# Kernel tuning notes

Hardware: AMD Instinct MI355X
Metric: run time of the kernel (lower is better)

Reference implementation:

```python
import jax, jax.numpy as jnp
import numpy as np

DIM = 2048
H = 16        # num query heads
HK = 2        # num kv heads
D = DIM // H  # head_dim = 128
G = H // HK   # q heads per kv head = 8
SCALE = 1.0 / np.sqrt(D)


def setup_inputs() -> dict:
    key = jax.random.key(0)
    ks = jax.random.split(key, 9)
    xavier = lambda k, fi, fo: jax.random.uniform(k, (fi, fo), jnp.float32,
                                                  -np.sqrt(6.0 / (fi + fo)), np.sqrt(6.0 / (fi + fo)))
    return {
        "x": jax.random.normal(ks[0], (2, 2048, DIM), jnp.float32),
        "Wq": xavier(ks[1], DIM, H * D),  "bq": jnp.zeros((H * D,), jnp.float32),
        "Wk": xavier(ks[2], DIM, HK * D), "bk": jnp.zeros((HK * D,), jnp.float32),
        "Wv": xavier(ks[3], DIM, HK * D), "bv": jnp.zeros((HK * D,), jnp.float32),
        "Wo": xavier(ks[4], H * D, DIM),  "bo": jnp.zeros((DIM,), jnp.float32),
    }


def reference(x, Wq, bq, Wk, bk, Wv, bv, Wo, bo):
    B, T, C = x.shape
    # projections; q grouped as (kv_head, group) so repeat_interleave becomes a broadcast
    q = (x @ Wq + bq).reshape(B, T, HK, G, D)   # [B,T,Hk,G,D]
    k = (x @ Wk + bk).reshape(B, T, HK, D)      # [B,T,Hk,D]
    v = (x @ Wv + bv).reshape(B, T, HK, D)
    # scores: [B,Hk,G,Tq,Tk] — shared K broadcast across the G query heads per kv head
    scores = jnp.einsum('bqhgd,bshd->bhgqs', q, k) * SCALE
    scores = jnp.clip(scores, -100.0, 100.0)
    attn = jax.nn.softmax(scores, axis=-1)
    out = jnp.einsum('bhgqs,bshd->bqhgd', attn, v).reshape(B, T, H * D)
    return out @ Wo + bo
```

## Files before the change

### kernel.cpp

```cpp
#include <hip/hip_runtime.h>
#include <cstdint>

typedef __bf16 bf16x8 __attribute__((ext_vector_type(8)));
typedef float floatx4 __attribute__((ext_vector_type(4)));
typedef float floatx16 __attribute__((ext_vector_type(16)));
typedef unsigned short u16;
typedef unsigned int u32;

#define SCALE2 0.1275434297677098f
#define CLIP2  144.26950408889634f
#define DEFER  8.0f

__device__ __forceinline__ u16 f2bf(float f) {
  union { float f; u32 i; } v; v.f = f;
  u32 r = v.i + 0x7fffu + ((v.i >> 16) & 1u);
  return (u16)(r >> 16);
}

__device__ __forceinline__ u32 cvtpk(float lo, float hi) {
  u32 r;
  asm("v_cvt_pk_bf16_f32 %0, %1, %2" : "=v"(r) : "v"(lo), "v"(hi));
  return r;
}

__device__ __forceinline__ void gll16(const void* g, void* l) {
  __builtin_amdgcn_global_load_lds(
      (const __attribute__((address_space(1))) u32*)g,
      (__attribute__((address_space(3))) u32*)l, 16, 0, 0);
}

__global__ __launch_bounds__(256) void convert_bf16(
    const float* __restrict__ src, u16* __restrict__ dst, int n4) {
  int i = blockIdx.x * 256 + threadIdx.x;
  if (i >= n4) return;
  float4 v = ((const float4*)src)[i];
  ushort4 o;
  o.x = f2bf(v.x); o.y = f2bf(v.y); o.z = f2bf(v.z); o.w = f2bf(v.w);
  ((ushort4*)dst)[i] = o;
}

__global__ __launch_bounds__(256) void transpose_all(
    const float* __restrict__ Wq, const float* __restrict__ Wk,
    const float* __restrict__ Wv, const float* __restrict__ Wo,
    u16* __restrict__ Wqkv_t, u16* __restrict__ Wot) {
  __shared__ u16 tile[32][33];
  const int k0 = blockIdx.x * 32, ny = blockIdx.y;
  const float* src; int ld, nb, n0; u16* dst;
  if (ny < 80) {
    n0 = ny * 32; dst = Wqkv_t;
    if (n0 < 2048)      { src = Wq; ld = 2048; nb = n0; }
    else if (n0 < 2304) { src = Wk; ld = 256;  nb = n0 - 2048; }
    else                { src = Wv; ld = 256;  nb = n0 - 2304; }
  } else {
    n0 = (ny - 80) * 32; dst = Wot; src = Wo; ld = 2048; nb = n0;
  }
  const int tx = threadIdx.x, ty = threadIdx.y;
#pragma unroll
  for (int i = 0; i < 4; i++) {
    int k = ty + i * 8;
    tile[k][tx] = f2bf(src[(size_t)(k0 + k) * ld + nb + tx]);
  }
  __syncthreads();
#pragma unroll
  for (int i = 0; i < 4; i++) {
    int n = ty + i * 8;
    dst[(size_t)(n0 + n) * 2048 + k0 + tx] = tile[tx][n];
  }
}

template <int EPI, int NWG>
__global__ __launch_bounds__(256) void gemm_bt(
    const u16* __restrict__ A, const u16* __restrict__ Bt,
    const float* __restrict__ bias0, const float* __restrict__ bias1,
    const float* __restrict__ bias2,
    u16* __restrict__ out0, u16* __restrict__ out1, u16* __restrict__ out2,
    float* __restrict__ outf,
    int M, int N, int K) {
  __shared__ u16 As[2][128][32];
  __shared__ u16 Bs[2][128][32];
  const int tid  = threadIdx.x;
  const int w    = tid >> 6, L = tid & 63, ln = L & 15, quad = L >> 4;
  const int lin  = blockIdx.x + gridDim.x * blockIdx.y;
  const int swz  = (lin & 7) * (NWG >> 3) + (lin >> 3);
  const int bx   = swz % gridDim.x, by = swz / gridDim.x;
  const int m0   = by * 128, n0 = bx * 128;
  const int mw   = (w & 1) * 64, nw = (w >> 1) * 64;
  const int sr = w * 32 + (L >> 2), sc = (L & 3) * 8;
  const u16* ga = &A [(size_t)(m0 + sr) * K + sc];
  const u16* gb = &Bt[(size_t)(n0 + sr) * K + sc];
  floatx4 acc[4][4] = {};
  const int nk = K >> 5;

  gll16(ga, &As[0][w * 32][0]);
  gll16(ga + (size_t)16 * K, &As[0][w * 32 + 16][0]);
  gll16(gb, &Bs[0][w * 32][0]);
  gll16(gb + (size_t)16 * K, &Bs[0][w * 32 + 16][0]);

  for (int i = 0; i < nk; i++) {
    const int cur = i & 1;
    __syncthreads();
    if (i + 1 < nk) {
      const int kt = (i + 1) << 5;
      gll16(ga + kt, &As[cur ^ 1][w * 32][0]);
      gll16(ga + (size_t)16 * K + kt, &As[cur ^ 1][w * 32 + 16][0]);
      gll16(gb + kt, &Bs[cur ^ 1][w * 32][0]);
      gll16(gb + (size_t)16 * K + kt, &Bs[cur ^ 1][w * 32 + 16][0]);
    }
    bf16x8 af[4], bf[4];
#pragma unroll
    for (int mb = 0; mb < 4; mb++) af[mb] = *(const bf16x8*)&As[cur][mw + mb * 16 + ln][quad * 8];
#pragma unroll
    for (int nb = 0; nb < 4; nb++) bf[nb] = *(const bf16x8*)&Bs[cur][nw + nb * 16 + ln][quad * 8];
#pragma unroll
    for (int mb = 0; mb < 4; mb++)
#pragma unroll
      for (int nb = 0; nb < 4; nb++)
        acc[mb][nb] = __builtin_amdgcn_mfma_f32_16x16x32_bf16(af[mb], bf[nb], acc[mb][nb], 0, 0, 0);
  }

#pragma unroll
  for (int mb = 0; mb < 4; mb++) {
#pragma unroll
    for (int nb = 0; nb < 4; nb++) {
#pragma unroll
      for (int r = 0; r < 4; r++) {
        const int m = m0 + mw + mb * 16 + quad * 4 + r;
        const int n = n0 + nw + nb * 16 + ln;
        float v = acc[mb][nb][r];
        if constexpr (EPI == 0) {
          if (n < 2048) {
            v = (v + bias0[n]) * SCALE2;
            out0[(size_t)m * 2048 + n] = f2bf(v);
          } else if (n < 2304) {
            const int j = n - 2048;
            v += bias1[j];
            out1[(size_t)m * 256 + j] = f2bf(v);
          } else {
            const int j = n - 2304;
            v += bias2[j];
            const int b = m >> 11, t = m & 2047;
            out2[((size_t)(b * 256 + j)) * 2048 + t] = f2bf(v);
          }
        } else {
          v += bias0[n];
          outf[(size_t)m * (size_t)N + n] = v;
        }
      }
    }
  }
}

__global__ __launch_bounds__(256, 2) void attn_kernel(
    const u16* __restrict__ Q, const u16* __restrict__ K,
    const u16* __restrict__ Vt, u16* __restrict__ O) {
  __shared__ u16 Ksh[2][16 * 512];
  __shared__ u16 Vsh[2][16 * 512];
  const int tid = threadIdx.x;
  const int w = tid >> 6, L = tid & 63;
  const int ln = L & 31, hf = L >> 5;
  const int qt = blockIdx.x, h = blockIdx.y, b = blockIdx.z;
  const int hk = h >> 3;
  const size_t qrow0 = (size_t)b * 2048 + qt * 128 + w * 32;

  const u16* Kbase = K + (size_t)b * 2048 * 256 + hk * 128;
  const u16* Vbase = Vt + (size_t)(b * 2 + hk) * 128 * 2048;

  const u16* gK[4];
  const u16* gV[4];
#pragma unroll
  for (int j = 0; j < 4; j++) {
    const int fK = 4 * w + j, mb = fK >> 3, kc = fK & 7;
    gK[j] = Kbase + (size_t)(mb * 32 + ln) * 256 + kc * 16 + hf * 8;
    const int fV = 4 * w + j, db = fV >> 2, ks = fV & 3;
    gV[j] = Vbase + (size_t)(db * 32 + ln) * 2048 + ks * 16 + hf * 8;
  }

  bf16x8 qf[8];
#pragma unroll
  for (int kc = 0; kc < 8; kc++)
    qf[kc] = *(const bf16x8*)&Q[(qrow0 + ln) * 2048 + h * 128 + kc * 16 + hf * 8];

  floatx16 oT[4] = {};
  float mrow = -1e30f, lrow = 0.f;

  auto issue = [&](int tile, int bufi) {
#pragma unroll
    for (int j = 0; j < 4; j++) {
      gll16(gK[j] + (size_t)tile * 64 * 256, &Ksh[bufi][(4 * w + j) * 512]);
      gll16(gV[j] + (size_t)tile * 64,       &Vsh[bufi][(4 * w + j) * 512]);
    }
  };

  auto qkt = [&](floatx16 (&sf)[2], const u16* kb) {
#pragma unroll
    for (int r = 0; r < 16; r++) { sf[0][r] = 0.f; sf[1][r] = 0.f; }
#pragma unroll
    for (int kc = 0; kc < 8; kc++) {
#pragma unroll
      for (int mb = 0; mb < 2; mb++) {
        bf16x8 kf = *(const bf16x8*)&kb[(mb * 8 + kc) * 512 + L * 8];
        sf[mb] = __builtin_amdgcn_mfma_f32_32x32x16_bf16(kf, qf[kc], sf[mb], 0, 0, 0);
      }
    }
  };

  auto softmax = [&](floatx16 (&sf)[2]) {
#pragma unroll
    for (int mb = 0; mb < 2; mb++)
#pragma unroll
      for (int r = 0; r < 16; r++)
        sf[mb][r] = __builtin_amdgcn_fmed3f(sf[mb][r], -CLIP2, CLIP2);
    float t16[16];
#pragma unroll
    for (int r = 0; r < 16; r++) t16[r] = fmaxf(sf[0][r], sf[1][r]);
#pragma unroll
    for (int d = 8; d >= 1; d >>= 1)
#pragma unroll
      for (int r = 0; r < d; r++) t16[r] = fmaxf(t16[r], t16[r + d]);
    const float mx = fmaxf(t16[0], __shfl_xor(t16[0], 32));
    const bool need = __ballot(mx > mrow + DEFER) != 0;
    float mn = mrow, alpha = 1.f;
    if (need) {
      mn = fmaxf(mrow, mx);
      alpha = __builtin_amdgcn_exp2f(mrow - mn);
      mrow = mn;
    }
#pragma unroll
    for (int mb = 0; mb < 2; mb++)
#pragma unroll
      for (int r = 0; r < 16; r++)
        sf[mb][r] = __builtin_amdgcn_exp2f(sf[mb][r] - mn);
    float s16[16];
#pragma unroll
    for (int r = 0; r < 16; r++) s16[r] = sf[0][r] + sf[1][r];
#pragma unroll
    for (int d = 8; d >= 1; d >>= 1)
#pragma unroll
      for (int r = 0; r < d; r++) s16[r] += s16[r + d];
    const float s = s16[0] + __shfl_xor(s16[0], 32);
    if (need) {
      lrow = lrow * alpha + s;
#pragma unroll
      for (int db = 0; db < 4; db++)
#pragma unroll
        for (int r = 0; r < 16; r++) oT[db][r] *= alpha;
    } else {
      lrow += s;
    }
  };

  auto pv = [&](floatx16 (&sf)[2], const u16* vb) {
#pragma unroll
    for (int ks = 0; ks < 4; ks++) {
      const int mb = ks >> 1, s8 = (ks & 1) * 8;
      u32 cA0 = cvtpk(sf[mb][s8 + 0], sf[mb][s8 + 1]);
      u32 cA1 = cvtpk(sf[mb][s8 + 2], sf[mb][s8 + 3]);
      u32 cB0 = cvtpk(sf[mb][s8 + 4], sf[mb][s8 + 5]);
      u32 cB1 = cvtpk(sf[mb][s8 + 6], sf[mb][s8 + 7]);
      asm("v_permlane32_swap_b32 %0, %1" : "+v"(cA0), "+v"(cB0));
      asm("v_permlane32_swap_b32 %0, %1" : "+v"(cA1), "+v"(cB1));
      union { u32 u[4]; bf16x8 v; } pb;
      pb.u[0] = cA0; pb.u[1] = cA1; pb.u[2] = cB0; pb.u[3] = cB1;
#pragma unroll
      for (int db = 0; db < 4; db++) {
        bf16x8 vf = *(const bf16x8*)&vb[(db * 4 + ks) * 512 + L * 8];
        oT[db] = __builtin_amdgcn_mfma_f32_32x32x16_bf16(vf, pb.v, oT[db], 0, 0, 0);
      }
    }
  };

  floatx16 sfA[2], sfB[2];

  issue(0, 0);
  __syncthreads();
  issue(1, 1);
  qkt(sfA, &Ksh[0][0]);

  for (int t = 0; t < 32; t += 2) {
    softmax(sfA);
    __syncthreads();
    __builtin_amdgcn_s_setprio(1);
    qkt(sfB, &Ksh[1][0]);
    pv(sfA, &Vsh[0][0]);
    __builtin_amdgcn_s_setprio(0);
    __syncthreads();
    if (t + 2 < 32) issue(t + 2, 0);
    softmax(sfB);
    __syncthreads();
    __builtin_amdgcn_s_setprio(1);
    if (t + 2 < 32) qkt(sfA, &Ksh[0][0]);
    pv(sfB, &Vsh[1][0]);
    __builtin_amdgcn_s_setprio(0);
    __syncthreads();
    if (t + 3 < 32) issue(t + 3, 1);
  }

  const float inv = 1.f / lrow;
  u16* orow = O + (qrow0 + ln) * 2048 + h * 128;
#pragma unroll
  for (int db = 0; db < 4; db++) {
#pragma unroll
    for (int g = 0; g < 4; g++) {
      uint2 st;
      st.x = cvtpk(oT[db][g * 4 + 0] * inv, oT[db][g * 4 + 1] * inv);
      st.y = cvtpk(oT[db][g * 4 + 2] * inv, oT[db][g * 4 + 3] * inv);
      *(uint2*)&orow[db * 32 + g * 8 + hf * 4] = st;
    }
  }
}

extern "C" void kernel_launch(void* const* d_in, const int* in_sizes, int n_in,
                              void* d_out, int out_size, void* d_ws, size_t ws_size,
                              hipStream_t stream) {
  const float* x  = (const float*)d_in[0];
  const float* Wq = (const float*)d_in[1];
  const float* bq = (const float*)d_in[2];
  const float* Wk = (const float*)d_in[3];
  const float* bk = (const float*)d_in[4];
  const float* Wv = (const float*)d_in[5];
  const float* bv = (const float*)d_in[6];
  const float* Wo = (const float*)d_in[7];
  const float* bo = (const float*)d_in[8];
  float* out = (float*)d_out;

  char* ws = (char*)d_ws;
  u16* xb     = (u16*)(ws);
  u16* Ob     = (u16*)(ws);
  u16* Wqkv_t = (u16*)(ws + 16777216);
  u16* Wot    = (u16*)(ws + 27262976);
  u16* Qb     = (u16*)(ws + 35651584);
  u16* Kb     = (u16*)(ws + 52428800);
  u16* Vtb    = (u16*)(ws + 54525952);
  (void)in_sizes; (void)n_in; (void)out_size; (void)ws_size;

  convert_bf16<<<8192, 256, 0, stream>>>(x, xb, 2097152);

  transpose_all<<<dim3(64, 144), dim3(32, 8), 0, stream>>>(
      Wq, Wk, Wv, Wo, Wqkv_t, Wot);

  gemm_bt<0, 640><<<dim3(20, 32), 256, 0, stream>>>(
      xb, Wqkv_t, bq, bk, bv, Qb, Kb, Vtb, nullptr, 4096, 2560, 2048);

  attn_kernel<<<dim3(16, 16, 2), 256, 0, stream>>>(Qb, Kb, Vtb, Ob);

  gemm_bt<1, 512><<<dim3(16, 32), 256, 0, stream>>>(
      Ob, Wot, bo, nullptr, nullptr, nullptr, nullptr, nullptr, out, 4096, 2048, 2048);
}
```

Before: 321.0 us.

## Triple-buffer GEMM LDS tiles with MFMA-fragment layout and vmcnt-based barriers

Changes the projection GEMM mainloop from double to triple buffering, issuing loads two K-steps ahead and waiting with s_waitcnt vmcnt(4) plus a raw barrier instead of a full __syncthreads. It also lays out LDS tiles in per-16-row fragment order, so each lane reads a contiguous 16 bytes at L*8, which avoids bank conflicts on fragment reads. The aim is to hide global load latency and cut LDS read stalls. In exchange it uses more shared memory, which may reduce occupancy, and the hand-written waitcnt counts must be correct for the loads to complete before use.

After: 374.4 us. 1.17x slower.

```diff
diff --git a/kernel.cpp b/kernel.cpp
--- a/kernel.cpp
+++ b/kernel.cpp
@@ -28,6 +28,12 @@
       (const __attribute__((address_space(1))) u32*)g,
       (__attribute__((address_space(3))) u32*)l, 16, 0, 0);
 }
+
+#define VMBAR(N)                                                   \
+  do {                                                             \
+    asm volatile("s_waitcnt vmcnt(" #N ")" ::: "memory");          \
+    __builtin_amdgcn_s_barrier();                                  \
+  } while (0)
 
 __global__ __launch_bounds__(256) void convert_bf16(
     const float* __restrict__ src, u16* __restrict__ dst, int n4) {
@@ -76,8 +82,8 @@
     u16* __restrict__ out0, u16* __restrict__ out1, u16* __restrict__ out2,
     float* __restrict__ outf,
     int M, int N, int K) {
-  __shared__ u16 As[2][128][32];
-  __shared__ u16 Bs[2][128][32];
+  __shared__ u16 As[3][4096];
+  __shared__ u16 Bs[3][4096];
   const int tid  = threadIdx.x;
   const int w    = tid >> 6, L = tid & 63, ln = L & 15, quad = L >> 4;
   const int lin  = blockIdx.x + gridDim.x * blockIdx.y;
@@ -85,32 +91,56 @@
   const int bx   = swz % gridDim.x, by = swz / gridDim.x;
   const int m0   = by * 128, n0 = bx * 128;
   const int mw   = (w & 1) * 64, nw = (w >> 1) * 64;
-  const int sr = w * 32 + (L >> 2), sc = (L & 3) * 8;
-  const u16* ga = &A [(size_t)(m0 + sr) * K + sc];
-  const u16* gb = &Bt[(size_t)(n0 + sr) * K + sc];
+  const int hk8 = quad * 8;
+  const u16* gA[2];
+  const u16* gB[2];
+#pragma unroll
+  for (int j = 0; j < 2; j++) {
+    gA[j] = &A [(size_t)(m0 + (2 * w + j) * 16 + ln) * K + hk8];
+    gB[j] = &Bt[(size_t)(n0 + (2 * w + j) * 16 + ln) * K + hk8];
+  }
   floatx4 acc[4][4] = {};
   const int nk = K >> 5;
 
-  gll16(ga, &As[0][w * 32][0]);
-  gll16(ga + (size_t)16 * K, &As[0][w * 32 + 16][0]);
-  gll16(gb, &Bs[0][w * 32][0]);
-  gll16(gb + (size_t)16 * K, &Bs[0][w * 32 + 16][0]);
-
-  for (int i = 0; i < nk; i++) {
-    const int cur = i & 1;
-    __syncthreads();
-    if (i + 1 < nk) {
-      const int kt = (i + 1) << 5;
-      gll16(ga + kt, &As[cur ^ 1][w * 32][0]);
-      gll16(ga + (size_t)16 * K + kt, &As[cur ^ 1][w * 32 + 16][0]);
-      gll16(gb + kt, &Bs[cur ^ 1][w * 32][0]);
-      gll16(gb + (size_t)16 * K + kt, &Bs[cur ^ 1][w * 32 + 16][0]);
-    }
+  auto issue = [&](int i, int ib) {
+    const size_t kt = (size_t)i * 32;
+#pragma unroll
+    for (int j = 0; j < 2; j++) {
+      gll16(gA[j] + kt, &As[ib][(2 * w + j) << 9]);
+      gll16(gB[j] + kt, &Bs[ib][(2 * w + j) << 9]);
+    }
+  };
+
+  issue(0, 0);
+  issue(1, 1);
+  int cb = 0;
+  for (int t = 0; t < nk - 1; t++) {
+    VMBAR(4);
+    int ib = cb - 1; if (ib < 0) ib = 2;
+    if (t + 2 < nk) issue(t + 2, ib);
     bf16x8 af[4], bf[4];
 #pragma unroll
-    for (int mb = 0; mb < 4; mb++) af[mb] = *(const bf16x8*)&As[cur][mw + mb * 16 + ln][quad * 8];
-#pragma unroll
-    for (int nb = 0; nb < 4; nb++) bf[nb] = *(const bf16x8*)&Bs[cur][nw + nb * 16 + ln][quad * 8];
+    for (int mb = 0; mb < 4; mb++)
+      af[mb] = *(const bf16x8*)&As[cb][(((w & 1) * 4 + mb) << 9) + (L << 3)];
+#pragma unroll
+    for (int nb = 0; nb < 4; nb++)
+      bf[nb] = *(const bf16x8*)&Bs[cb][(((w >> 1) * 4 + nb) << 9) + (L << 3)];
+#pragma unroll
+    for (int mb = 0; mb < 4; mb++)
+#pragma unroll
+      for (int nb = 0; nb < 4; nb++)
+        acc[mb][nb] = __builtin_amdgcn_mfma_f32_16x16x32_bf16(af[mb], bf[nb], acc[mb][nb], 0, 0, 0);
+    cb = (cb == 2) ? 0 : cb + 1;
+  }
+  VMBAR(0);
+  {
+    bf16x8 af[4], bf[4];
+#pragma unroll
+    for (int mb = 0; mb < 4; mb++)
+      af[mb] = *(const bf16x8*)&As[cb][(((w & 1) * 4 + mb) << 9) + (L << 3)];
+#pragma unroll
+    for (int nb = 0; nb < 4; nb++)
+      bf[nb] = *(const bf16x8*)&Bs[cb][(((w >> 1) * 4 + nb) << 9) + (L << 3)];
 #pragma unroll
     for (int mb = 0; mb < 4; mb++)
 #pragma unroll
```

## Triple-buffer GEMM LDS tiles with partial vmcnt waits for deeper prefetch

Applied to the files above, without the earlier changes.

Changes the projection GEMM's K-loop from double to triple LDS buffering. Two tiles are kept in flight, and each step waits with s_waitcnt vmcnt(4) so only the oldest tile must land before the barrier, not all outstanding loads. This is meant to hide global-to-LDS latency behind the MFMA work. It raises LDS use per block by half, which could lower occupancy, and it depends on vmcnt counting the async LDS loads correctly.

Result: no change. 320.9 us (-0.0%).

```diff
diff --git a/kernel.cpp b/kernel.cpp
--- a/kernel.cpp
+++ b/kernel.cpp
@@ -28,6 +28,12 @@
       (const __attribute__((address_space(1))) u32*)g,
       (__attribute__((address_space(3))) u32*)l, 16, 0, 0);
 }
+
+#define VMBAR(N)                                                   \
+  do {                                                             \
+    asm volatile("s_waitcnt vmcnt(" #N ")" ::: "memory");          \
+    __builtin_amdgcn_s_barrier();                                  \
+  } while (0)
 
 __global__ __launch_bounds__(256) void convert_bf16(
     const float* __restrict__ src, u16* __restrict__ dst, int n4) {
@@ -76,8 +82,8 @@
     u16* __restrict__ out0, u16* __restrict__ out1, u16* __restrict__ out2,
     float* __restrict__ outf,
     int M, int N, int K) {
-  __shared__ u16 As[2][128][32];
-  __shared__ u16 Bs[2][128][32];
+  __shared__ u16 As[3][128][32];
+  __shared__ u16 Bs[3][128][32];
   const int tid  = threadIdx.x;
   const int w    = tid >> 6, L = tid & 63, ln = L & 15, quad = L >> 4;
   const int lin  = blockIdx.x + gridDim.x * blockIdx.y;
@@ -91,32 +97,38 @@
   floatx4 acc[4][4] = {};
   const int nk = K >> 5;
 
-  gll16(ga, &As[0][w * 32][0]);
-  gll16(ga + (size_t)16 * K, &As[0][w * 32 + 16][0]);
-  gll16(gb, &Bs[0][w * 32][0]);
-  gll16(gb + (size_t)16 * K, &Bs[0][w * 32 + 16][0]);
-
-  for (int i = 0; i < nk; i++) {
-    const int cur = i & 1;
-    __syncthreads();
-    if (i + 1 < nk) {
-      const int kt = (i + 1) << 5;
-      gll16(ga + kt, &As[cur ^ 1][w * 32][0]);
-      gll16(ga + (size_t)16 * K + kt, &As[cur ^ 1][w * 32 + 16][0]);
-      gll16(gb + kt, &Bs[cur ^ 1][w * 32][0]);
-      gll16(gb + (size_t)16 * K + kt, &Bs[cur ^ 1][w * 32 + 16][0]);
-    }
+  auto issue = [&](int i, int ib) {
+    const size_t kt = (size_t)i << 5;
+    gll16(ga + kt,                  &As[ib][w * 32][0]);
+    gll16(ga + (size_t)16 * K + kt, &As[ib][w * 32 + 16][0]);
+    gll16(gb + kt,                  &Bs[ib][w * 32][0]);
+    gll16(gb + (size_t)16 * K + kt, &Bs[ib][w * 32 + 16][0]);
+  };
+  auto compute = [&](int cb) {
     bf16x8 af[4], bf[4];
 #pragma unroll
-    for (int mb = 0; mb < 4; mb++) af[mb] = *(const bf16x8*)&As[cur][mw + mb * 16 + ln][quad * 8];
-#pragma unroll
-    for (int nb = 0; nb < 4; nb++) bf[nb] = *(const bf16x8*)&Bs[cur][nw + nb * 16 + ln][quad * 8];
+    for (int mb = 0; mb < 4; mb++) af[mb] = *(const bf16x8*)&As[cb][mw + mb * 16 + ln][quad * 8];
+#pragma unroll
+    for (int nb = 0; nb < 4; nb++) bf[nb] = *(const bf16x8*)&Bs[cb][nw + nb * 16 + ln][quad * 8];
 #pragma unroll
     for (int mb = 0; mb < 4; mb++)
 #pragma unroll
       for (int nb = 0; nb < 4; nb++)
         acc[mb][nb] = __builtin_amdgcn_mfma_f32_16x16x32_bf16(af[mb], bf[nb], acc[mb][nb], 0, 0, 0);
-  }
+  };
+
+  issue(0, 0);
+  issue(1, 1);
+  int cb = 0;
+  for (int t = 0; t < nk - 1; t++) {
+    VMBAR(4);
+    int ib = cb - 1; if (ib < 0) ib = 2;
+    if (t + 2 < nk) issue(t + 2, ib);
+    compute(cb);
+    cb = (cb == 2) ? 0 : cb + 1;
+  }
+  VMBAR(0);
+  compute(cb);
 
 #pragma unroll
   for (int mb = 0; mb < 4; mb++) {
```

## Double GEMM K-tile to 64 with XOR-swizzled LDS layout

Applied to the files above, without the earlier changes.

Doubles the K depth of each shared-memory tile in the projection/output GEMM from 32 to 64, which halves the number of barrier-separated iterations. It also stores each row's 16-byte slots XOR-swizzled by row index so that fragment reads avoid LDS bank conflicts. LDS use doubles to 64 KB per block, which may reduce occupancy, and the global-load addressing becomes more complex.

After: 337.0 us. 5.0% more time.

```diff
diff --git a/kernel.cpp b/kernel.cpp
--- a/kernel.cpp
+++ b/kernel.cpp
@@ -76,46 +76,53 @@
     u16* __restrict__ out0, u16* __restrict__ out1, u16* __restrict__ out2,
     float* __restrict__ outf,
     int M, int N, int K) {
-  __shared__ u16 As[2][128][32];
-  __shared__ u16 Bs[2][128][32];
+  __shared__ u16 As[2][128][64];
+  __shared__ u16 Bs[2][128][64];
   const int tid  = threadIdx.x;
   const int w    = tid >> 6, L = tid & 63, ln = L & 15, quad = L >> 4;
+  const int lrow = L >> 3;
+  const int lslot = (L & 7) ^ lrow;
   const int lin  = blockIdx.x + gridDim.x * blockIdx.y;
   const int swz  = (lin & 7) * (NWG >> 3) + (lin >> 3);
   const int bx   = swz % gridDim.x, by = swz / gridDim.x;
   const int m0   = by * 128, n0 = bx * 128;
   const int mw   = (w & 1) * 64, nw = (w >> 1) * 64;
-  const int sr = w * 32 + (L >> 2), sc = (L & 3) * 8;
-  const u16* ga = &A [(size_t)(m0 + sr) * K + sc];
-  const u16* gb = &Bt[(size_t)(n0 + sr) * K + sc];
+  const u16* ga = &A [(size_t)(m0 + w * 32 + lrow) * K + lslot * 8];
+  const u16* gb = &Bt[(size_t)(n0 + w * 32 + lrow) * K + lslot * 8];
   floatx4 acc[4][4] = {};
-  const int nk = K >> 5;
-
-  gll16(ga, &As[0][w * 32][0]);
-  gll16(ga + (size_t)16 * K, &As[0][w * 32 + 16][0]);
-  gll16(gb, &Bs[0][w * 32][0]);
-  gll16(gb + (size_t)16 * K, &Bs[0][w * 32 + 16][0]);
-
-  for (int i = 0; i < nk; i++) {
-    const int cur = i & 1;
-    __syncthreads();
-    if (i + 1 < nk) {
-      const int kt = (i + 1) << 5;
-      gll16(ga + kt, &As[cur ^ 1][w * 32][0]);
-      gll16(ga + (size_t)16 * K + kt, &As[cur ^ 1][w * 32 + 16][0]);
-      gll16(gb + kt, &Bs[cur ^ 1][w * 32][0]);
-      gll16(gb + (size_t)16 * K + kt, &Bs[cur ^ 1][w * 32 + 16][0]);
-    }
-    bf16x8 af[4], bf[4];
-#pragma unroll
-    for (int mb = 0; mb < 4; mb++) af[mb] = *(const bf16x8*)&As[cur][mw + mb * 16 + ln][quad * 8];
-#pragma unroll
-    for (int nb = 0; nb < 4; nb++) bf[nb] = *(const bf16x8*)&Bs[cur][nw + nb * 16 + ln][quad * 8];
-#pragma unroll
-    for (int mb = 0; mb < 4; mb++)
-#pragma unroll
-      for (int nb = 0; nb < 4; nb++)
-        acc[mb][nb] = __builtin_amdgcn_mfma_f32_16x16x32_bf16(af[mb], bf[nb], acc[mb][nb], 0, 0, 0);
+  const int nk = K >> 6;
+
+  auto issue = [&](int i, int ib) {
+    const size_t kt = (size_t)i << 6;
+#pragma unroll
+    for (int j = 0; j < 4; j++) {
+      gll16(ga + (size_t)(j * 8) * K + kt, &As[ib][w * 32 + j * 8][0]);
+      gll16(gb + (size_t)(j * 8) * K + kt, &Bs[ib][w * 32 + j * 8][0]);
+    }
+  };
+  auto compute = [&](int cb) {
+#pragma unroll
+    for (int s = 0; s < 2; s++) {
+      const int so = (((s << 2) | quad) ^ (ln & 7)) * 8;
+      bf16x8 af[4], bf[4];
+#pragma unroll
+      for (int mb = 0; mb < 4; mb++) af[mb] = *(const bf16x8*)&As[cb][mw + mb * 16 + ln][so];
+#pragma unroll
+      for (int nb = 0; nb < 4; nb++) bf[nb] = *(const bf16x8*)&Bs[cb][nw + nb * 16 + ln][so];
+#pragma unroll
+      for (int mb = 0; mb < 4; mb++)
+#pragma unroll
+        for (int nb = 0; nb < 4; nb++)
+          acc[mb][nb] = __builtin_amdgcn_mfma_f32_16x16x32_bf16(af[mb], bf[nb], acc[mb][nb], 0, 0, 0);
+    }
+  };
+
+  issue(0, 0);
+  for (int t = 0; t < nk; t++) {
+    const int cur = t & 1;
+    __syncthreads();
+    if (t + 1 < nk) issue(t + 1, cur ^ 1);
+    compute(cur);
   }
 
 #pragma unroll
```
